# Performance work log

Measured on AMD Instinct MI355X. Metric: run time of the kernel, lower is better.

Reference implementation:

```python
import jax, jax.numpy as jnp
import numpy as np

N = 100000   # nodes
E = 1000000  # edges
DIN = 128    # atom_in_features
DE = 16      # edge_attr_dim
H = 128      # hidden width (preprocess/cheb/postprocess)
K = 3        # Chebyshev order
EPS = 1e-5


def setup_inputs() -> dict:
    key = jax.random.key(0)
    ks = jax.random.split(key, 16)
    s = 0.02
    return {
        "x": jax.random.normal(ks[0], (N, DIN), jnp.float32),
        "edge_index": jax.random.randint(ks[1], (2, E), 0, N),
        "edge_attr": jax.random.normal(ks[2], (E, DE), jnp.float32),
        # AtomEdgeInteraction linear: (DIN+DE) -> H
        "w_int": jax.random.normal(ks[3], (DIN + DE, H), jnp.float32) * s,
        "b_int": jnp.zeros((H,), jnp.float32),
        # preprocess layer 1: Linear + BatchNorm + ReLU
        "w_pre": jax.random.normal(ks[4], (H, H), jnp.float32) * s,
        "b_pre": jnp.zeros((H,), jnp.float32),
        "g_pre": jnp.ones((H,), jnp.float32),
        "be_pre": jnp.zeros((H,), jnp.float32),
        # ChebConv layers: weight [K, in, out] + bias
        "cheb1_w": jax.random.normal(ks[5], (K, H, H), jnp.float32) * s,
        "cheb1_b": jnp.zeros((H,), jnp.float32),
        "cheb2_w": jax.random.normal(ks[6], (K, H, H), jnp.float32) * s,
        "cheb2_b": jnp.zeros((H,), jnp.float32),
        # postprocess: Linear + BatchNorm + ReLU
        "w_post": jax.random.normal(ks[7], (H, H), jnp.float32) * s,
        "b_post": jnp.zeros((H,), jnp.float32),
        "g_post": jnp.ones((H,), jnp.float32),
        "be_post": jnp.zeros((H,), jnp.float32),
        # output layer H -> 1
        "w_out": jax.random.normal(ks[8], (H, 1), jnp.float32) * s,
        "b_out": jnp.zeros((1,), jnp.float32),
    }


def _bn(z, g, b):
    # BatchNorm1d, training-mode batch statistics (biased variance, like torch)
    m = z.mean(0)
    v = ((z - m) ** 2).mean(0)
    return g * (z - m) * jax.lax.rsqrt(v + EPS) + b


def _cheb(h, W, b, row, col, norm):
    # ChebConv with sym normalization, lambda_max=2 => L_hat = -D^{-1/2} A D^{-1/2}
    def lhat(z):
        return jax.ops.segment_sum(norm[:, None] * z[row], col, num_segments=N)

    Tx0 = h
    out = Tx0 @ W[0]
    Tx1 = lhat(Tx0)
    out = out + Tx1 @ W[1]
    for k in range(2, W.shape[0]):
        Tx2 = 2.0 * lhat(Tx1) - Tx0
        out = out + Tx2 @ W[k]
        Tx0, Tx1 = Tx1, Tx2
    return out + b


def reference(x, edge_index, edge_attr,
              w_int, b_int,
              w_pre, b_pre, g_pre, be_pre,
              cheb1_w, cheb1_b, cheb2_w, cheb2_b,
              w_post, b_post, g_post, be_post,
              w_out, b_out):
    row, col = edge_index[0], edge_index[1]
    ones_e = jnp.ones((E,), x.dtype)

    # AtomEdgeInteraction: gather -> concat -> linear -> scatter_mean over col
    comb = jnp.concatenate([x[row], edge_attr], axis=-1)  # [E, DIN+DE]
    upd = comb @ w_int + b_int                             # [E, H]
    cnt = jax.ops.segment_sum(ones_e, col, num_segments=N)
    h = jax.ops.segment_sum(upd, col, num_segments=N) / jnp.clip(cnt, 1.0)[:, None]

    # preprocess layer 1 (Linear + BN + ReLU; dropout rate 0)
    h = jax.nn.relu(_bn(h @ w_pre + b_pre, g_pre, be_pre))

    # sym-normalized edge coefficients for scaled Laplacian
    deg = jax.ops.segment_sum(ones_e, row, num_segments=N)
    dis = jnp.where(deg > 0, jax.lax.rsqrt(jnp.maximum(deg, 1.0)), 0.0)
    norm = -dis[row] * dis[col]  # [E]

    h = jax.nn.relu(_cheb(h, cheb1_w, cheb1_b, row, col, norm))
    h = jax.nn.relu(_cheb(h, cheb2_w, cheb2_b, row, col, norm))

    # postprocess (Linear + BN + ReLU)
    h = jax.nn.relu(_bn(h @ w_post + b_post, g_post, be_post))

    # output layer, squeeze(-1) -> [N]
    return (h @ w_out + b_out).squeeze(-1)
```

## Files before the change

### kernel.cpp

```cpp
#include <hip/hip_runtime.h>
#include <hip/hip_bf16.h>

using u16 = unsigned short;
using u32 = unsigned int;

#define NN 100000
#define NE 1000000

typedef __attribute__((ext_vector_type(8))) short bfrag;
typedef __attribute__((ext_vector_type(4))) float ffrag;

#define BF16ONE2 0x3F803F80u

__device__ __forceinline__ float bf2f(u16 u) { return __uint_as_float(((u32)u) << 16); }
__device__ __forceinline__ u16 f2bf(float f) {
  u32 x = __float_as_uint(f);
  return (u16)((x + 0x7fffu + ((x >> 16) & 1u)) >> 16);
}
__device__ __forceinline__ float rdv(const void* p, long i, int f) {
  return f ? bf2f(((const u16*)p)[i]) : ((const float*)p)[i];
}
__device__ __forceinline__ void acc8(float* a, uint4 v, float w) {
  a[0] = fmaf(w, __uint_as_float(v.x << 16), a[0]);
  a[1] = fmaf(w, __uint_as_float(v.x & 0xffff0000u), a[1]);
  a[2] = fmaf(w, __uint_as_float(v.y << 16), a[2]);
  a[3] = fmaf(w, __uint_as_float(v.y & 0xffff0000u), a[3]);
  a[4] = fmaf(w, __uint_as_float(v.z << 16), a[4]);
  a[5] = fmaf(w, __uint_as_float(v.z & 0xffff0000u), a[5]);
  a[6] = fmaf(w, __uint_as_float(v.w << 16), a[6]);
  a[7] = fmaf(w, __uint_as_float(v.w & 0xffff0000u), a[7]);
}

#define OWXT 0
#define OWPRE 16384
#define OWD1 32768
#define OW11 49152
#define OV21 65536
#define OWD2 81920
#define OW12 98304
#define OV22 114688
#define OWPOST 131072
#define OWET 147456

struct PrepArgs { const void* in[16]; };

__global__ void k_prep(PrepArgs a, const u32* __restrict__ gp, u16* __restrict__ wq,
                       float* __restrict__ wf) {
  int t = blockIdx.x * 256 + threadIdx.x;
  int f = (gp[0] == BF16ONE2) ? 1 : 0;
  if (t < 16384) {
    int o = t >> 7, k = t & 127;
    int ko = k * 128 + o;
    int ok = o * 128 + k;
    wq[OWXT + ok] = f2bf(rdv(a.in[0], ko, f));
    wq[OWPRE + ok] = f2bf(rdv(a.in[2], ko, f));
    float c0 = rdv(a.in[6], ko, f);
    float c1 = rdv(a.in[6], 16384 + ko, f);
    float c2 = rdv(a.in[6], 32768 + ko, f);
    wq[OWD1 + ok] = f2bf(c0 - c2);
    wq[OW11 + ok] = f2bf(c1);
    wq[OV21 + ok] = f2bf(2.f * c2);
    float d0 = rdv(a.in[8], ko, f);
    float d1 = rdv(a.in[8], 16384 + ko, f);
    float d2 = rdv(a.in[8], 32768 + ko, f);
    wq[OWD2 + ok] = f2bf(d0 - d2);
    wq[OW12 + ok] = f2bf(d1);
    wq[OV22 + ok] = f2bf(2.f * d2);
    wq[OWPOST + ok] = f2bf(rdv(a.in[10], ko, f));
  }
  if (t < 4096) {
    int o = t >> 5, k = t & 31;
    wq[OWET + o * 32 + k] = (k < 16) ? f2bf(rdv(a.in[0], (long)(128 + k) * 128 + o, f)) : (u16)0;
  }
  if (t < 1281) {
    int s = t >> 7, j = t & 127;
    const int map[11] = {1, 3, 4, 5, 7, 9, 11, 12, 13, 14, 15};
    wf[t] = rdv(a.in[map[s]], j, f);
  }
}

__global__ void k_hist(const int* __restrict__ ei, int* cnt, int* deg) {
  int e = blockIdx.x * 256 + threadIdx.x;
  if (e >= NE) return;
  atomicAdd(&deg[ei[e]], 1);
  atomicAdd(&cnt[ei[NE + e]], 1);
}

__global__ void k_scan1(const int* __restrict__ cnt, int* off, int* bsum) {
  __shared__ int s[1024];
  int t = threadIdx.x;
  int g = blockIdx.x * 1024 + t;
  int v = (g < NN) ? cnt[g] : 0;
  s[t] = v;
  __syncthreads();
  for (int st = 1; st < 1024; st <<= 1) {
    int x = (t >= st) ? s[t - st] : 0;
    __syncthreads();
    s[t] += x;
    __syncthreads();
  }
  if (g < NN) off[g] = s[t] - v;
  if (t == 1023) bsum[blockIdx.x] = s[t];
}

__global__ void k_scan23(int* off, const int* __restrict__ bsum,
                         const int* __restrict__ deg, float* __restrict__ dis, int nb) {
  __shared__ int s[128];
  int t = threadIdx.x;
  int v = 0;
  if (t < 128) {
    v = (t < nb) ? bsum[t] : 0;
    s[t] = v;
  }
  __syncthreads();
  for (int st = 1; st < 128; st <<= 1) {
    int x = (t >= st && t < 128) ? s[t - st] : 0;
    __syncthreads();
    if (t < 128) s[t] += x;
    __syncthreads();
  }
  if (t < 128) s[t] -= v;
  __syncthreads();
  int pre = s[blockIdx.x];
  int g = blockIdx.x * 1024 + t;
  if (g < NN) {
    off[g] += pre;
    int d = deg[g];
    dis[g] = d > 0 ? rsqrtf((float)d) : 0.f;
  }
  if (g == 0) off[NN] = NE;
}

__global__ void k_place(const int* __restrict__ ei, const int* __restrict__ off,
                        int* cur, int* crow, int* ceid) {
  int e = blockIdx.x * 256 + threadIdx.x;
  if (e >= NE) return;
  int r = ei[e], c = ei[NE + e];
  int p = off[c] + atomicAdd(&cur[c], 1);
  crow[p] = r;
  ceid[p] = e;
}

__global__ __launch_bounds__(256) void k_spmm(const u16* __restrict__ src,
                                              u16* __restrict__ dst,
                                              const int* __restrict__ off,
                                              const int* __restrict__ crow,
                                              const float* __restrict__ cnorm,
                                              const u16* __restrict__ G, int relu) {
  int t = threadIdx.x;
  int node = blockIdx.x * 8 + (t >> 5);
  if (node >= NN) return;
  int l = t & 31;
  int half = l >> 4;
  int c = (l & 15) * 8;
  int p0 = off[node], p1 = off[node + 1];
  float a[8];
#pragma unroll
  for (int j = 0; j < 8; j++) a[j] = 0.f;
  const u16* sp = src + c;
  if (cnorm) {
    int p = p0 + half;
    for (; p + 6 < p1; p += 8) {
      int r0 = crow[p], r1 = crow[p + 2], r2 = crow[p + 4], r3 = crow[p + 6];
      float w0 = cnorm[p], w1 = cnorm[p + 2], w2 = cnorm[p + 4], w3 = cnorm[p + 6];
      uint4 v0 = *(const uint4*)(sp + (long)r0 * 128);
      uint4 v1 = *(const uint4*)(sp + (long)r1 * 128);
      uint4 v2 = *(const uint4*)(sp + (long)r2 * 128);
      uint4 v3 = *(const uint4*)(sp + (long)r3 * 128);
      acc8(a, v0, w0);
      acc8(a, v1, w1);
      acc8(a, v2, w2);
      acc8(a, v3, w3);
    }
    for (; p < p1; p += 2) {
      acc8(a, *(const uint4*)(sp + (long)crow[p] * 128), cnorm[p]);
    }
  } else {
    int p = p0 + half;
    for (; p + 6 < p1; p += 8) {
      int r0 = crow[p], r1 = crow[p + 2], r2 = crow[p + 4], r3 = crow[p + 6];
      uint4 v0 = *(const uint4*)(sp + (long)r0 * 128);
      uint4 v1 = *(const uint4*)(sp + (long)r1 * 128);
      uint4 v2 = *(const uint4*)(sp + (long)r2 * 128);
      uint4 v3 = *(const uint4*)(sp + (long)r3 * 128);
      acc8(a, v0, 1.f);
      acc8(a, v1, 1.f);
      acc8(a, v2, 1.f);
      acc8(a, v3, 1.f);
    }
    for (; p < p1; p += 2) acc8(a, *(const uint4*)(sp + (long)crow[p] * 128), 1.f);
  }
#pragma unroll
  for (int j = 0; j < 8; j++) a[j] += __shfl_xor(a[j], 16);
  if (half) return;
  if (G) acc8(a, *(const uint4*)(G + (long)node * 128 + c), 1.f);
  if (relu) {
#pragma unroll
    for (int j = 0; j < 8; j++) a[j] = fmaxf(a[j], 0.f);
  }
  uint4 o;
  o.x = (u32)f2bf(a[0]) | ((u32)f2bf(a[1]) << 16);
  o.y = (u32)f2bf(a[2]) | ((u32)f2bf(a[3]) << 16);
  o.z = (u32)f2bf(a[4]) | ((u32)f2bf(a[5]) << 16);
  o.w = (u32)f2bf(a[6]) | ((u32)f2bf(a[7]) << 16);
  *(uint4*)(dst + (long)node * 128 + c) = o;
}

__global__ __launch_bounds__(256) void k_asum(const void* __restrict__ eattr,
                                              const u32* __restrict__ gp,
                                              u16* __restrict__ asum,
                                              const int* __restrict__ off,
                                              const int* __restrict__ ceid,
                                              const int* __restrict__ crow,
                                              const float* __restrict__ dis,
                                              float* __restrict__ cnorm) {
  int t = blockIdx.x * 256 + threadIdx.x;
  int node = t >> 4;
  if (node >= NN) return;
  int j = t & 15;
  int p0 = off[node], p1 = off[node + 1];
  float ndis = -dis[node];
  for (int p = p0 + j; p < p1; p += 16) cnorm[p] = ndis * dis[crow[p]];
  float a = 0.f;
  if (gp[0] == BF16ONE2) {
    const u16* e16 = (const u16*)eattr;
    int p = p0;
    for (; p + 4 <= p1; p += 4) {
      float v0 = bf2f(e16[(long)ceid[p] * 16 + j]);
      float v1 = bf2f(e16[(long)ceid[p + 1] * 16 + j]);
      float v2 = bf2f(e16[(long)ceid[p + 2] * 16 + j]);
      float v3 = bf2f(e16[(long)ceid[p + 3] * 16 + j]);
      a += v0 + v1 + v2 + v3;
    }
    for (; p < p1; p++) a += bf2f(e16[(long)ceid[p] * 16 + j]);
  } else {
    const float* e32 = (const float*)eattr;
    int p = p0;
    for (; p + 4 <= p1; p += 4) {
      float v0 = e32[(long)ceid[p] * 16 + j];
      float v1 = e32[(long)ceid[p + 1] * 16 + j];
      float v2 = e32[(long)ceid[p + 2] * 16 + j];
      float v3 = e32[(long)ceid[p + 3] * 16 + j];
      a += v0 + v1 + v2 + v3;
    }
    for (; p < p1; p++) a += e32[(long)ceid[p] * 16 + j];
  }
  asum[(long)node * 16 + j] = f2bf(a);
}

struct MArgs {
  const void* A0; const u16* W0T; int a0raw;
  const u16* A1; const u16* W1T;
  const u16* W2T; u16* out2;
  const float* bias;
  u16* out;
  const u32* gp;
  float* part;
};

#define ASTRIDE 136
#define ESTRIDE 132

template <int DUAL, int K0, int ROWS>
__global__ __launch_bounds__(256) void k_mgemm(MArgs m) {
  constexpr int RT = ROWS / 16;
  constexpr int TPR = 256 / ROWS;
  constexpr int SEGW = K0 / TPR;
  constexpr int NKB0 = K0 / 32;
  __shared__ __align__(16) u16 sA[ROWS * ASTRIDE];
  int tid = threadIdx.x;
  int wv = tid >> 6, lane = tid & 63;
  int col16 = lane & 15, quad = lane >> 4;
  int r0 = blockIdx.x * ROWS;

  ffrag acc[RT * 2];
#pragma unroll
  for (int i = 0; i < RT * 2; i++)
#pragma unroll
    for (int g = 0; g < 4; g++) acc[i][g] = 0.f;

  {
    int row = tid / TPR, seg = tid % TPR;
    int ra = r0 + row;
    if (ra >= NN) ra = NN - 1;
    bool f32a = m.a0raw && (m.gp[0] != BF16ONE2);
    if (f32a) {
      const float* gs = (const float*)m.A0 + (long)ra * K0 + seg * SEGW;
      u32* lp = (u32*)(sA + row * ASTRIDE + seg * SEGW);
#pragma unroll
      for (int e = 0; e < SEGW / 8; e++) {
        float4 v0 = *(const float4*)(gs + e * 8);
        float4 v1 = *(const float4*)(gs + e * 8 + 4);
        lp[e * 4 + 0] = (u32)f2bf(v0.x) | ((u32)f2bf(v0.y) << 16);
        lp[e * 4 + 1] = (u32)f2bf(v0.z) | ((u32)f2bf(v0.w) << 16);
        lp[e * 4 + 2] = (u32)f2bf(v1.x) | ((u32)f2bf(v1.y) << 16);
        lp[e * 4 + 3] = (u32)f2bf(v1.z) | ((u32)f2bf(v1.w) << 16);
      }
    } else {
      const u16* gs = (const u16*)m.A0 + (long)ra * K0 + seg * SEGW;
      uint4* lp = (uint4*)(sA + row * ASTRIDE + seg * SEGW);
#pragma unroll
      for (int e = 0; e < SEGW / 8; e++) lp[e] = *(const uint4*)(gs + e * 8);
    }
  }
  bfrag b0[2][NKB0];
#pragma unroll
  for (int c = 0; c < 2; c++)
#pragma unroll
    for (int kb = 0; kb < NKB0; kb++)
      b0[c][kb] = *(const bfrag*)(m.W0T + (long)(wv * 32 + c * 16 + col16) * K0 + kb * 32 + quad * 8);
  __syncthreads();
#pragma unroll
  for (int kb = 0; kb < NKB0; kb++)
#pragma unroll
    for (int rt = 0; rt < RT; rt++) {
      bfrag af = *(const bfrag*)(sA + (rt * 16 + col16) * ASTRIDE + kb * 32 + quad * 8);
      acc[rt * 2 + 0] = __builtin_amdgcn_mfma_f32_16x16x32_bf16(af, b0[0][kb], acc[rt * 2 + 0], 0, 0, 0);
      acc[rt * 2 + 1] = __builtin_amdgcn_mfma_f32_16x16x32_bf16(af, b0[1][kb], acc[rt * 2 + 1], 0, 0, 0);
    }

  ffrag acc2[DUAL ? RT * 2 : 1];
  if constexpr (DUAL) {
#pragma unroll
    for (int i = 0; i < RT * 2; i++)
#pragma unroll
      for (int g = 0; g < 4; g++) acc2[i][g] = 0.f;
    __syncthreads();
    {
      int row = tid / TPR, seg = tid % TPR;
      int ra = r0 + row;
      if (ra >= NN) ra = NN - 1;
      const u16* gs = m.A1 + (long)ra * 128 + seg * SEGW;
      uint4* lp = (uint4*)(sA + row * ASTRIDE + seg * SEGW);
#pragma unroll
      for (int e = 0; e < SEGW / 8; e++) lp[e] = *(const uint4*)(gs + e * 8);
    }
    bfrag b1[2][4], b2[2][4];
#pragma unroll
    for (int c = 0; c < 2; c++)
#pragma unroll
      for (int kb = 0; kb < 4; kb++) {
        b1[c][kb] = *(const bfrag*)(m.W1T + (long)(wv * 32 + c * 16 + col16) * 128 + kb * 32 + quad * 8);
        b2[c][kb] = *(const bfrag*)(m.W2T + (long)(wv * 32 + c * 16 + col16) * 128 + kb * 32 + quad * 8);
      }
    __syncthreads();
#pragma unroll
    for (int kb = 0; kb < 4; kb++)
#pragma unroll
      for (int rt = 0; rt < RT; rt++) {
        bfrag af = *(const bfrag*)(sA + (rt * 16 + col16) * ASTRIDE + kb * 32 + quad * 8);
        acc[rt * 2 + 0] = __builtin_amdgcn_mfma_f32_16x16x32_bf16(af, b1[0][kb], acc[rt * 2 + 0], 0, 0, 0);
        acc[rt * 2 + 1] = __builtin_amdgcn_mfma_f32_16x16x32_bf16(af, b1[1][kb], acc[rt * 2 + 1], 0, 0, 0);
        acc2[rt * 2 + 0] = __builtin_amdgcn_mfma_f32_16x16x32_bf16(af, b2[0][kb], acc2[rt * 2 + 0], 0, 0, 0);
        acc2[rt * 2 + 1] = __builtin_amdgcn_mfma_f32_16x16x32_bf16(af, b2[1][kb], acc2[rt * 2 + 1], 0, 0, 0);
      }
  }

  __syncthreads();
#pragma unroll
  for (int rt = 0; rt < RT; rt++)
#pragma unroll
    for (int c = 0; c < 2; c++) {
      int col = wv * 32 + c * 16 + col16;
      float bj = m.bias ? m.bias[col] : 0.f;
#pragma unroll
      for (int g = 0; g < 4; g++)
        sA[(rt * 16 + quad * 4 + g) * ESTRIDE + col] = f2bf(acc[rt * 2 + c][g] + bj);
    }
  __syncthreads();
  {
    constexpr int CPT = 128 / TPR;
    int rr = tid / TPR, d = tid % TPR;
    int rowg = r0 + rr;
    if (rowg < NN) {
      const u16* sp2 = sA + rr * ESTRIDE + d * CPT;
      uint4* o = (uint4*)(m.out + (long)rowg * 128 + d * CPT);
#pragma unroll
      for (int e = 0; e < CPT / 8; e++) {
        const uint2* s2 = (const uint2*)(sp2 + e * 8);
        uint2 lo = s2[0], hi = s2[1];
        o[e] = make_uint4(lo.x, lo.y, hi.x, hi.y);
      }
    }
  }
  if (m.part) {
    __shared__ float ps[256], pq[256];
    int col = tid & 127, hf = tid >> 7;
    float s = 0.f, q = 0.f;
#pragma unroll
    for (int r = 0; r < ROWS / 2; r++) {
      int rr = hf * (ROWS / 2) + r;
      if (r0 + rr < NN) {
        float v = bf2f(sA[rr * ESTRIDE + col]);
        s += v;
        q += v * v;
      }
    }
    ps[tid] = s;
    pq[tid] = q;
    __syncthreads();
    if (tid < 128) {
      m.part[(long)blockIdx.x * 256 + tid] = ps[tid] + ps[tid + 128];
      m.part[(long)blockIdx.x * 256 + 128 + tid] = pq[tid] + pq[tid + 128];
    }
  }
  if constexpr (DUAL) {
    __syncthreads();
#pragma unroll
    for (int rt = 0; rt < RT; rt++)
#pragma unroll
      for (int c = 0; c < 2; c++) {
        int col = wv * 32 + c * 16 + col16;
#pragma unroll
        for (int g = 0; g < 4; g++)
          sA[(rt * 16 + quad * 4 + g) * ESTRIDE + col] = f2bf(acc2[rt * 2 + c][g]);
      }
    __syncthreads();
    constexpr int CPT = 128 / TPR;
    int rr = tid / TPR, d = tid % TPR;
    int rowg = r0 + rr;
    if (rowg < NN) {
      const u16* sp2 = sA + rr * ESTRIDE + d * CPT;
      uint4* o = (uint4*)(m.out2 + (long)rowg * 128 + d * CPT);
#pragma unroll
      for (int e = 0; e < CPT / 8; e++) {
        const uint2* s2 = (const uint2*)(sp2 + e * 8);
        uint2 lo = s2[0], hi = s2[1];
        o[e] = make_uint4(lo.x, lo.y, hi.x, hi.y);
      }
    }
  }
}

__global__ __launch_bounds__(256) void k_etpre(const u16* __restrict__ asum,
                                               const u16* __restrict__ Wet,
                                               const u16* __restrict__ Wpre,
                                               const float* __restrict__ b_int,
                                               const float* __restrict__ b_pre,
                                               const u16* __restrict__ G,
                                               const int* __restrict__ cnt,
                                               u16* __restrict__ out, float* part) {
  __shared__ __align__(16) u16 sA[64 * ASTRIDE];
  int tid = threadIdx.x;
  int wv = tid >> 6, lane = tid & 63;
  int col16 = lane & 15, quad = lane >> 4;
  int r0 = blockIdx.x * 64;

  {
    int row = tid >> 2, seg = tid & 3;
    int ra = r0 + row;
    if (ra >= NN) ra = NN - 1;
    if (seg < 2) {
      *(uint4*)(sA + row * ASTRIDE + seg * 8) = *(const uint4*)(asum + (long)ra * 16 + seg * 8);
    } else {
      *(uint4*)(sA + row * ASTRIDE + seg * 8) = make_uint4(0, 0, 0, 0);
    }
  }
  bfrag be[2];
#pragma unroll
  for (int c = 0; c < 2; c++)
    be[c] = *(const bfrag*)(Wet + (long)(wv * 32 + c * 16 + col16) * 32 + quad * 8);
  __syncthreads();
  ffrag acc[8];
#pragma unroll
  for (int i = 0; i < 8; i++)
#pragma unroll
    for (int g = 0; g < 4; g++) acc[i][g] = 0.f;
#pragma unroll
  for (int rt = 0; rt < 4; rt++) {
    bfrag af = *(const bfrag*)(sA + (rt * 16 + col16) * ASTRIDE + quad * 8);
    acc[rt * 2 + 0] = __builtin_amdgcn_mfma_f32_16x16x32_bf16(af, be[0], acc[rt * 2 + 0], 0, 0, 0);
    acc[rt * 2 + 1] = __builtin_amdgcn_mfma_f32_16x16x32_bf16(af, be[1], acc[rt * 2 + 1], 0, 0, 0);
  }
  __syncthreads();
#pragma unroll
  for (int rt = 0; rt < 4; rt++)
#pragma unroll
    for (int c = 0; c < 2; c++) {
      int col = wv * 32 + c * 16 + col16;
      float bj = b_int[col];
#pragma unroll
      for (int g = 0; g < 4; g++) {
        int r = r0 + rt * 16 + quad * 4 + g;
        float v = acc[rt * 2 + c][g];
        int cc = 0;
        if (r < NN) {
          v += bf2f(G[(long)r * 128 + col]);
          cc = cnt[r];
        }
        v = (v + (float)cc * bj) / (float)(cc > 1 ? cc : 1);
        sA[(rt * 16 + quad * 4 + g) * ASTRIDE + col] = f2bf(v);
      }
    }
  bfrag b1[2][4];
#pragma unroll
  for (int c = 0; c < 2; c++)
#pragma unroll
    for (int kb = 0; kb < 4; kb++)
      b1[c][kb] = *(const bfrag*)(Wpre + (long)(wv * 32 + c * 16 + col16) * 128 + kb * 32 + quad * 8);
  __syncthreads();
  ffrag a2[8];
#pragma unroll
  for (int i = 0; i < 8; i++)
#pragma unroll
    for (int g = 0; g < 4; g++) a2[i][g] = 0.f;
#pragma unroll
  for (int kb = 0; kb < 4; kb++)
#pragma unroll
    for (int rt = 0; rt < 4; rt++) {
      bfrag af = *(const bfrag*)(sA + (rt * 16 + col16) * ASTRIDE + kb * 32 + quad * 8);
      a2[rt * 2 + 0] = __builtin_amdgcn_mfma_f32_16x16x32_bf16(af, b1[0][kb], a2[rt * 2 + 0], 0, 0, 0);
      a2[rt * 2 + 1] = __builtin_amdgcn_mfma_f32_16x16x32_bf16(af, b1[1][kb], a2[rt * 2 + 1], 0, 0, 0);
    }
  __syncthreads();
#pragma unroll
  for (int rt = 0; rt < 4; rt++)
#pragma unroll
    for (int c = 0; c < 2; c++) {
      int col = wv * 32 + c * 16 + col16;
      float bj = b_pre[col];
#pragma unroll
      for (int g = 0; g < 4; g++)
        sA[(rt * 16 + quad * 4 + g) * ESTRIDE + col] = f2bf(a2[rt * 2 + c][g] + bj);
    }
  __syncthreads();
  {
    int rr = tid >> 2, d = tid & 3;
    int rowg = r0 + rr;
    if (rowg < NN) {
      const u16* sp2 = sA + rr * ESTRIDE + d * 32;
      uint4* o = (uint4*)(out + (long)rowg * 128 + d * 32);
#pragma unroll
      for (int e = 0; e < 4; e++) {
        const uint2* s2 = (const uint2*)(sp2 + e * 8);
        uint2 lo = s2[0], hi = s2[1];
        o[e] = make_uint4(lo.x, lo.y, hi.x, hi.y);
      }
    }
  }
  {
    __shared__ float ps[256], pq[256];
    int col = tid & 127, hf = tid >> 7;
    float s = 0.f, q = 0.f;
#pragma unroll
    for (int r = 0; r < 32; r++) {
      int rr = hf * 32 + r;
      if (r0 + rr < NN) {
        float v = bf2f(sA[rr * ESTRIDE + col]);
        s += v;
        q += v * v;
      }
    }
    ps[tid] = s;
    pq[tid] = q;
    __syncthreads();
    if (tid < 128) {
      part[(long)blockIdx.x * 256 + tid] = ps[tid] + ps[tid + 128];
      part[(long)blockIdx.x * 256 + 128 + tid] = pq[tid] + pq[tid + 128];
    }
  }
}

__global__ void k_redfin(const float* __restrict__ part, const float* __restrict__ gamma,
                         const float* __restrict__ beta, float* ab, int nblk) {
  int tid = threadIdx.x;
  int col = blockIdx.x * 16 + (tid & 15);
  int ch = tid >> 4;
  float s = 0.f, q = 0.f;
  for (int b = ch; b < nblk; b += 16) {
    s += part[(long)b * 256 + col];
    q += part[(long)b * 256 + 128 + col];
  }
  __shared__ float sh[256], qh[256];
  sh[tid] = s;
  qh[tid] = q;
  __syncthreads();
  if (tid < 16) {
    float ts = 0.f, tq = 0.f;
#pragma unroll
    for (int i = 0; i < 16; i++) {
      ts += sh[i * 16 + tid];
      tq += qh[i * 16 + tid];
    }
    int j = blockIdx.x * 16 + tid;
    float m = ts * (1.f / (float)NN);
    float v = fmaxf(tq * (1.f / (float)NN) - m * m, 0.f);
    float a = gamma[j] * rsqrtf(v + 1e-5f);
    ab[j] = a;
    ab[128 + j] = beta[j] - m * a;
  }
}

__global__ void k_bnrelu(const u16* __restrict__ z, u16* __restrict__ out,
                         const float* __restrict__ ab) {
  long idx = (long)blockIdx.x * 256 + threadIdx.x;
  long t = idx * 2;
  if (t >= (long)NN * 128) return;
  int col = (int)(t & 127);
  u32 v = *(const u32*)(z + t);
  float f0 = fmaxf(__uint_as_float(v << 16) * ab[col] + ab[128 + col], 0.f);
  float f1 = fmaxf(__uint_as_float(v & 0xffff0000u) * ab[col + 1] + ab[129 + col], 0.f);
  *(u32*)(out + t) = (u32)f2bf(f0) | ((u32)f2bf(f1) << 16);
}

__global__ void k_out(const u16* __restrict__ z, const float* __restrict__ ab,
                      const float* __restrict__ wout, const float* __restrict__ bout,
                      const u32* __restrict__ gp, void* __restrict__ y) {
  int node = blockIdx.x * 4 + (threadIdx.x >> 6);
  if (node >= NN) return;
  int lane = threadIdx.x & 63;
  float s = 0.f;
#pragma unroll
  for (int c = lane; c < 128; c += 64) {
    float zz = bf2f(z[(long)node * 128 + c]);
    float h = fmaxf(ab[c] * zz + ab[128 + c], 0.f);
    s += h * wout[c];
  }
#pragma unroll
  for (int o = 32; o > 0; o >>= 1) s += __shfl_down(s, o);
  if (lane == 0) {
    float r = s + bout[0];
    if (gp[0] == BF16ONE2) ((u16*)y)[node] = f2bf(r);
    else ((float*)y)[node] = r;
  }
}

extern "C" void kernel_launch(void* const* d_in, const int* in_sizes, int n_in,
                              void* d_out, int out_size, void* d_ws, size_t ws_size,
                              hipStream_t stream) {
  const void* x = d_in[0];
  const int* ei = (const int*)d_in[1];
  const void* eattr = d_in[2];
  const u32* gp = (const u32*)d_in[7];
  (void)in_sizes; (void)n_in; (void)out_size; (void)ws_size;

  char* w = (char*)d_ws;
  size_t p = 0;
  auto alloc = [&](size_t b) { size_t r = p; p += (b + 255) & ~(size_t)255; return r; };
  size_t o_cnt = alloc((size_t)NN * 4);
  size_t o_deg = alloc((size_t)NN * 4);
  size_t o_cur = alloc((size_t)NN * 4);
  size_t o_zero_end = p;
  size_t o_dis = alloc((size_t)NN * 4);
  size_t o_off = alloc((size_t)(NN + 1) * 4);
  size_t o_bsum = alloc(1024 * 4);
  size_t o_ab = alloc(512 * 4);
  size_t o_wq = alloc((size_t)151552 * 2);
  size_t o_wf = alloc((size_t)1281 * 4);
  size_t o_crow = alloc((size_t)NE * 4);
  size_t o_cnrm = alloc((size_t)NE * 4);
  size_t o_asum = alloc((size_t)NN * 16 * 2);
  size_t o_part = alloc((size_t)1563 * 256 * 4);
  size_t o_Bx = alloc((size_t)NN * 128 * 2);
  size_t o_Bt = alloc((size_t)NN * 128 * 2);

  int* cnt = (int*)(w + o_cnt);
  int* deg = (int*)(w + o_deg);
  int* cur = (int*)(w + o_cur);
  float* dis = (float*)(w + o_dis);
  int* off = (int*)(w + o_off);
  int* bsum = (int*)(w + o_bsum);
  float* abA = (float*)(w + o_ab);
  float* abB = abA + 256;
  u16* wq = (u16*)(w + o_wq);
  float* wf = (float*)(w + o_wf);
  int* crow = (int*)(w + o_crow);
  float* cnrm = (float*)(w + o_cnrm);
  u16* asum = (u16*)(w + o_asum);
  float* part = (float*)(w + o_part);
  u16* Bx = (u16*)(w + o_Bx);
  u16* Bt = (u16*)(w + o_Bt);
  int* ceid = (int*)Bt;

  hipMemsetAsync(w + o_cnt, 0, o_zero_end - o_cnt, stream);

  int gE = (NE + 255) / 256;
  int nb = (NN + 1023) / 1024;
  int gS = (NN + 7) / 8;
  int gG1 = (NN + 127) / 128;
  int gG2 = (NN + 63) / 64;

  {
    PrepArgs a;
    for (int i = 0; i < 16; i++) a.in[i] = d_in[3 + i];
    k_prep<<<64, 256, 0, stream>>>(a, gp, wq, wf);
  }

  k_hist<<<gE, 256, 0, stream>>>(ei, cnt, deg);
  k_scan1<<<nb, 1024, 0, stream>>>(cnt, off, bsum);
  k_scan23<<<nb, 1024, 0, stream>>>(off, bsum, deg, dis, nb);
  k_place<<<gE, 256, 0, stream>>>(ei, off, cur, crow, ceid);
  k_asum<<<(NN * 16 + 255) / 256, 256, 0, stream>>>(eattr, gp, asum, off, ceid, crow, dis, cnrm);

  {
    MArgs a = {};
    a.A0 = x; a.W0T = wq + OWXT; a.a0raw = 1;
    a.out = Bx; a.gp = gp;
    k_mgemm<0, 128, 128><<<gG1, 256, 0, stream>>>(a);
  }
  k_spmm<<<gS, 256, 0, stream>>>(Bx, Bt, off, crow, nullptr, nullptr, 0);
  k_etpre<<<gG2, 256, 0, stream>>>(asum, wq + OWET, wq + OWPRE, wf + 0, wf + 128,
                                   Bt, cnt, Bt, part);
  k_redfin<<<8, 256, 0, stream>>>(part, wf + 256, wf + 384, abA, gG2);
  k_bnrelu<<<(int)(((long)NN * 128 / 2 + 255) / 256), 256, 0, stream>>>(Bt, Bx, abA);

  k_spmm<<<gS, 256, 0, stream>>>(Bx, Bt, off, crow, cnrm, nullptr, 0);
  {
    MArgs a = {};
    a.A0 = Bx; a.W0T = wq + OWD1;
    a.A1 = Bt; a.W1T = wq + OW11;
    a.W2T = wq + OV21; a.out2 = Bt;
    a.bias = wf + 512; a.out = Bx; a.gp = gp;
    k_mgemm<1, 128, 64><<<gG2, 256, 0, stream>>>(a);
  }
  k_spmm<<<gS, 256, 0, stream>>>(Bt, Bx, off, crow, cnrm, Bx, 1);

  k_spmm<<<gS, 256, 0, stream>>>(Bx, Bt, off, crow, cnrm, nullptr, 0);
  {
    MArgs a = {};
    a.A0 = Bx; a.W0T = wq + OWD2;
    a.A1 = Bt; a.W1T = wq + OW12;
    a.W2T = wq + OV22; a.out2 = Bt;
    a.bias = wf + 640; a.out = Bx; a.gp = gp;
    k_mgemm<1, 128, 64><<<gG2, 256, 0, stream>>>(a);
  }
  k_spmm<<<gS, 256, 0, stream>>>(Bt, Bx, off, crow, cnrm, Bx, 1);

  {
    MArgs a = {};
    a.A0 = Bx; a.W0T = wq + OWPOST;
    a.bias = wf + 768; a.out = Bt; a.gp = gp; a.part = part;
    k_mgemm<0, 128, 128><<<gG1, 256, 0, stream>>>(a);
  }
  k_redfin<<<8, 256, 0, stream>>>(part, wf + 896, wf + 1024, abB, gG1);
  k_out<<<(NN + 3) / 4, 256, 0, stream>>>(Bt, abB, wf + 1152, wf + 1280, gp, d_out);
}
```

Baseline: 809.6 us.

## Fuse neighbor gather into Chebyshev and preprocess GEMM kernels

The sparse aggregation is moved inside the GEMM kernels. A new gather_lds helper accumulates neighbor rows straight into shared memory: unweighted for the interaction step in k_etpre, and weighted by cnorm for the second Chebyshev term in the new k_cheb. k_cheb takes the place of the earlier pattern of a dual GEMM, a write of an intermediate T1@W2 product, and a second gather with bias and relu. This removes one standalone sparse-aggregation launch per Chebyshev layer and one for the interaction step, along with their intermediate round trips through global memory. In exchange, each 16-thread group gathers four nodes one after another inside a GEMM-shaped block, which may lower memory-level parallelism for the irregular loads.

```diff
diff --git a/kernel.cpp b/kernel.cpp
--- a/kernel.cpp
+++ b/kernel.cpp
@@ -41,6 +41,9 @@
 #define OV22 114688
 #define OWPOST 131072
 #define OWET 147456
+
+#define ASTRIDE 136
+#define ESTRIDE 132
 
 struct PrepArgs { const void* in[16]; };
 
@@ -145,8 +148,7 @@
                                               u16* __restrict__ dst,
                                               const int* __restrict__ off,
                                               const int* __restrict__ crow,
-                                              const float* __restrict__ cnorm,
-                                              const u16* __restrict__ G, int relu) {
+                                              const float* __restrict__ cnorm) {
   int t = threadIdx.x;
   int node = blockIdx.x * 8 + (t >> 5);
   if (node >= NN) return;
@@ -158,52 +160,75 @@
 #pragma unroll
   for (int j = 0; j < 8; j++) a[j] = 0.f;
   const u16* sp = src + c;
-  if (cnorm) {
-    int p = p0 + half;
-    for (; p + 6 < p1; p += 8) {
-      int r0 = crow[p], r1 = crow[p + 2], r2 = crow[p + 4], r3 = crow[p + 6];
-      float w0 = cnorm[p], w1 = cnorm[p + 2], w2 = cnorm[p + 4], w3 = cnorm[p + 6];
-      uint4 v0 = *(const uint4*)(sp + (long)r0 * 128);
-      uint4 v1 = *(const uint4*)(sp + (long)r1 * 128);
-      uint4 v2 = *(const uint4*)(sp + (long)r2 * 128);
-      uint4 v3 = *(const uint4*)(sp + (long)r3 * 128);
-      acc8(a, v0, w0);
-      acc8(a, v1, w1);
-      acc8(a, v2, w2);
-      acc8(a, v3, w3);
-    }
-    for (; p < p1; p += 2) {
-      acc8(a, *(const uint4*)(sp + (long)crow[p] * 128), cnorm[p]);
-    }
-  } else {
-    int p = p0 + half;
-    for (; p + 6 < p1; p += 8) {
-      int r0 = crow[p], r1 = crow[p + 2], r2 = crow[p + 4], r3 = crow[p + 6];
-      uint4 v0 = *(const uint4*)(sp + (long)r0 * 128);
-      uint4 v1 = *(const uint4*)(sp + (long)r1 * 128);
-      uint4 v2 = *(const uint4*)(sp + (long)r2 * 128);
-      uint4 v3 = *(const uint4*)(sp + (long)r3 * 128);
-      acc8(a, v0, 1.f);
-      acc8(a, v1, 1.f);
-      acc8(a, v2, 1.f);
-      acc8(a, v3, 1.f);
-    }
-    for (; p < p1; p += 2) acc8(a, *(const uint4*)(sp + (long)crow[p] * 128), 1.f);
-  }
+  int p = p0 + half;
+  for (; p + 6 < p1; p += 8) {
+    int r0 = crow[p], r1 = crow[p + 2], r2 = crow[p + 4], r3 = crow[p + 6];
+    float w0 = cnorm[p], w1 = cnorm[p + 2], w2 = cnorm[p + 4], w3 = cnorm[p + 6];
+    uint4 v0 = *(const uint4*)(sp + (long)r0 * 128);
+    uint4 v1 = *(const uint4*)(sp + (long)r1 * 128);
+    uint4 v2 = *(const uint4*)(sp + (long)r2 * 128);
+    uint4 v3 = *(const uint4*)(sp + (long)r3 * 128);
+    acc8(a, v0, w0);
+    acc8(a, v1, w1);
+    acc8(a, v2, w2);
+    acc8(a, v3, w3);
+  }
+  for (; p < p1; p += 2) acc8(a, *(const uint4*)(sp + (long)crow[p] * 128), cnorm[p]);
 #pragma unroll
   for (int j = 0; j < 8; j++) a[j] += __shfl_xor(a[j], 16);
   if (half) return;
-  if (G) acc8(a, *(const uint4*)(G + (long)node * 128 + c), 1.f);
-  if (relu) {
-#pragma unroll
-    for (int j = 0; j < 8; j++) a[j] = fmaxf(a[j], 0.f);
-  }
   uint4 o;
   o.x = (u32)f2bf(a[0]) | ((u32)f2bf(a[1]) << 16);
   o.y = (u32)f2bf(a[2]) | ((u32)f2bf(a[3]) << 16);
   o.z = (u32)f2bf(a[4]) | ((u32)f2bf(a[5]) << 16);
   o.w = (u32)f2bf(a[6]) | ((u32)f2bf(a[7]) << 16);
   *(uint4*)(dst + (long)node * 128 + c) = o;
+}
+
+template <int WEIGHTED>
+__device__ __forceinline__ void gather_lds(u16* sA, const u16* __restrict__ src,
+                                           const int* __restrict__ off,
+                                           const int* __restrict__ crow,
+                                           const float* __restrict__ cnorm, int r0) {
+  int tid = threadIdx.x;
+  int grp = tid >> 4;
+  int c = (tid & 15) * 8;
+  const u16* sp = src + c;
+#pragma unroll
+  for (int i = 0; i < 4; i++) {
+    int nl = grp * 4 + i;
+    int node = r0 + nl;
+    float a[8];
+#pragma unroll
+    for (int j = 0; j < 8; j++) a[j] = 0.f;
+    if (node < NN) {
+      int p0 = off[node], p1 = off[node + 1];
+      int p = p0;
+      for (; p + 4 <= p1; p += 4) {
+        int r0i = crow[p], r1i = crow[p + 1], r2i = crow[p + 2], r3i = crow[p + 3];
+        float w0 = WEIGHTED ? cnorm[p] : 1.f;
+        float w1 = WEIGHTED ? cnorm[p + 1] : 1.f;
+        float w2 = WEIGHTED ? cnorm[p + 2] : 1.f;
+        float w3 = WEIGHTED ? cnorm[p + 3] : 1.f;
+        uint4 v0 = *(const uint4*)(sp + (long)r0i * 128);
+        uint4 v1 = *(const uint4*)(sp + (long)r1i * 128);
+        uint4 v2 = *(const uint4*)(sp + (long)r2i * 128);
+        uint4 v3 = *(const uint4*)(sp + (long)r3i * 128);
+        acc8(a, v0, w0);
+        acc8(a, v1, w1);
+        acc8(a, v2, w2);
+        acc8(a, v3, w3);
+      }
+      for (; p < p1; p++)
+        acc8(a, *(const uint4*)(sp + (long)crow[p] * 128), WEIGHTED ? cnorm[p] : 1.f);
+    }
+    uint4 o;
+    o.x = (u32)f2bf(a[0]) | ((u32)f2bf(a[1]) << 16);
+    o.y = (u32)f2bf(a[2]) | ((u32)f2bf(a[3]) << 16);
+    o.z = (u32)f2bf(a[4]) | ((u32)f2bf(a[5]) << 16);
+    o.w = (u32)f2bf(a[6]) | ((u32)f2bf(a[7]) << 16);
+    *(uint4*)(sA + nl * ASTRIDE + c) = o;
+  }
 }
 
 __global__ __launch_bounds__(256) void k_asum(const void* __restrict__ eattr,
@@ -250,23 +275,14 @@
 
 struct MArgs {
   const void* A0; const u16* W0T; int a0raw;
-  const u16* A1; const u16* W1T;
-  const u16* W2T; u16* out2;
   const float* bias;
   u16* out;
   const u32* gp;
   float* part;
 };
 
-#define ASTRIDE 136
-#define ESTRIDE 132
-
-template <int DUAL, int K0, int ROWS>
 __global__ __launch_bounds__(256) void k_mgemm(MArgs m) {
-  constexpr int RT = ROWS / 16;
-  constexpr int TPR = 256 / ROWS;
-  constexpr int SEGW = K0 / TPR;
-  constexpr int NKB0 = K0 / 32;
+  constexpr int ROWS = 128, RT = 8, TPR = 2, SEGW = 64;
   __shared__ __align__(16) u16 sA[ROWS * ASTRIDE];
   int tid = threadIdx.x;
   int wv = tid >> 6, lane = tid & 63;
@@ -285,7 +301,7 @@
     if (ra >= NN) ra = NN - 1;
     bool f32a = m.a0raw && (m.gp[0] != BF16ONE2);
     if (f32a) {
-      const float* gs = (const float*)m.A0 + (long)ra * K0 + seg * SEGW;
+      const float* gs = (const float*)m.A0 + (long)ra * 128 + seg * SEGW;
       u32* lp = (u32*)(sA + row * ASTRIDE + seg * SEGW);
 #pragma unroll
       for (int e = 0; e < SEGW / 8; e++) {
@@ -297,65 +313,27 @@
         lp[e * 4 + 3] = (u32)f2bf(v1.z) | ((u32)f2bf(v1.w) << 16);
       }
     } else {
-      const u16* gs = (const u16*)m.A0 + (long)ra * K0 + seg * SEGW;
+      const u16* gs = (const u16*)m.A0 + (long)ra * 128 + seg * SEGW;
       uint4* lp = (uint4*)(sA + row * ASTRIDE + seg * SEGW);
 #pragma unroll
       for (int e = 0; e < SEGW / 8; e++) lp[e] = *(const uint4*)(gs + e * 8);
     }
   }
-  bfrag b0[2][NKB0];
+  bfrag b0[2][4];
 #pragma unroll
   for (int c = 0; c < 2; c++)
 #pragma unroll
-    for (int kb = 0; kb < NKB0; kb++)
-      b0[c][kb] = *(const bfrag*)(m.W0T + (long)(wv * 32 + c * 16 + col16) * K0 + kb * 32 + quad * 8);
-  __syncthreads();
-#pragma unroll
-  for (int kb = 0; kb < NKB0; kb++)
+    for (int kb = 0; kb < 4; kb++)
+      b0[c][kb] = *(const bfrag*)(m.W0T + (long)(wv * 32 + c * 16 + col16) * 128 + kb * 32 + quad * 8);
+  __syncthreads();
+#pragma unroll
+  for (int kb = 0; kb < 4; kb++)
 #pragma unroll
     for (int rt = 0; rt < RT; rt++) {
       bfrag af = *(const bfrag*)(sA + (rt * 16 + col16) * ASTRIDE + kb * 32 + quad * 8);
       acc[rt * 2 + 0] = __builtin_amdgcn_mfma_f32_16x16x32_bf16(af, b0[0][kb], acc[rt * 2 + 0], 0, 0, 0);
       acc[rt * 2 + 1] = __builtin_amdgcn_mfma_f32_16x16x32_bf16(af, b0[1][kb], acc[rt * 2 + 1], 0, 0, 0);
     }
-
-  ffrag acc2[DUAL ? RT * 2 : 1];
-  if constexpr (DUAL) {
-#pragma unroll
-    for (int i = 0; i < RT * 2; i++)
-#pragma unroll
-      for (int g = 0; g < 4; g++) acc2[i][g] = 0.f;
-    __syncthreads();
-    {
-      int row = tid / TPR, seg = tid % TPR;
-      int ra = r0 + row;
-      if (ra >= NN) ra = NN - 1;
-      const u16* gs = m.A1 + (long)ra * 128 + seg * SEGW;
-      uint4* lp = (uint4*)(sA + row * ASTRIDE + seg * SEGW);
-#pragma unroll
-      for (int e = 0; e < SEGW / 8; e++) lp[e] = *(const uint4*)(gs + e * 8);
-    }
-    bfrag b1[2][4], b2[2][4];
-#pragma unroll
-    for (int c = 0; c < 2; c++)
-#pragma unroll
-      for (int kb = 0; kb < 4; kb++) {
-        b1[c][kb] = *(const bfrag*)(m.W1T + (long)(wv * 32 + c * 16 + col16) * 128 + kb * 32 + quad * 8);
-        b2[c][kb] = *(const bfrag*)(m.W2T + (long)(wv * 32 + c * 16 + col16) * 128 + kb * 32 + quad * 8);
-      }
-    __syncthreads();
-#pragma unroll
-    for (int kb = 0; kb < 4; kb++)
-#pragma unroll
-      for (int rt = 0; rt < RT; rt++) {
-        bfrag af = *(const bfrag*)(sA + (rt * 16 + col16) * ASTRIDE + kb * 32 + quad * 8);
-        acc[rt * 2 + 0] = __builtin_amdgcn_mfma_f32_16x16x32_bf16(af, b1[0][kb], acc[rt * 2 + 0], 0, 0, 0);
-        acc[rt * 2 + 1] = __builtin_amdgcn_mfma_f32_16x16x32_bf16(af, b1[1][kb], acc[rt * 2 + 1], 0, 0, 0);
-        acc2[rt * 2 + 0] = __builtin_amdgcn_mfma_f32_16x16x32_bf16(af, b2[0][kb], acc2[rt * 2 + 0], 0, 0, 0);
-        acc2[rt * 2 + 1] = __builtin_amdgcn_mfma_f32_16x16x32_bf16(af, b2[1][kb], acc2[rt * 2 + 1], 0, 0, 0);
-      }
-  }
-
   __syncthreads();
 #pragma unroll
   for (int rt = 0; rt < RT; rt++)
@@ -369,14 +347,13 @@
     }
   __syncthreads();
   {
-    constexpr int CPT = 128 / TPR;
     int rr = tid / TPR, d = tid % TPR;
     int rowg = r0 + rr;
     if (rowg < NN) {
-      const u16* sp2 = sA + rr * ESTRIDE + d * CPT;
-      uint4* o = (uint4*)(m.out + (long)rowg * 128 + d * CPT);
-#pragma unroll
-      for (int e = 0; e < CPT / 8; e++) {
+      const u16* sp2 = sA + rr * ESTRIDE + d * 64;
+      uint4* o = (uint4*)(m.out + (long)rowg * 128 + d * 64);
+#pragma unroll
+      for (int e = 0; e < 8; e++) {
         const uint2* s2 = (const uint2*)(sp2 + e * 8);
         uint2 lo = s2[0], hi = s2[1];
         o[e] = make_uint4(lo.x, lo.y, hi.x, hi.y);
@@ -388,8 +365,8 @@
     int col = tid & 127, hf = tid >> 7;
     float s = 0.f, q = 0.f;
 #pragma unroll
-    for (int r = 0; r < ROWS / 2; r++) {
-      int rr = hf * (ROWS / 2) + r;
+    for (int r = 0; r < 64; r++) {
+      int rr = hf * 64 + r;
       if (r0 + rr < NN) {
         float v = bf2f(sA[rr * ESTRIDE + col]);
         s += v;
@@ -404,40 +381,16 @@
       m.part[(long)blockIdx.x * 256 + 128 + tid] = pq[tid] + pq[tid + 128];
     }
   }
-  if constexpr (DUAL) {
-    __syncthreads();
-#pragma unroll
-    for (int rt = 0; rt < RT; rt++)
-#pragma unroll
-      for (int c = 0; c < 2; c++) {
-        int col = wv * 32 + c * 16 + col16;
-#pragma unroll
-        for (int g = 0; g < 4; g++)
-          sA[(rt * 16 + quad * 4 + g) * ESTRIDE + col] = f2bf(acc2[rt * 2 + c][g]);
-      }
-    __syncthreads();
-    constexpr int CPT = 128 / TPR;
-    int rr = tid / TPR, d = tid % TPR;
-    int rowg = r0 + rr;
-    if (rowg < NN) {
-      const u16* sp2 = sA + rr * ESTRIDE + d * CPT;
-      uint4* o = (uint4*)(m.out2 + (long)rowg * 128 + d * CPT);
-#pragma unroll
-      for (int e = 0; e < CPT / 8; e++) {
-        const uint2* s2 = (const uint2*)(sp2 + e * 8);
-        uint2 lo = s2[0], hi = s2[1];
-        o[e] = make_uint4(lo.x, lo.y, hi.x, hi.y);
-      }
-    }
-  }
-}
-
-__global__ __launch_bounds__(256) void k_etpre(const u16* __restrict__ asum,
+}
+
+__global__ __launch_bounds__(256) void k_etpre(const u16* __restrict__ Xg,
+                                               const u16* __restrict__ asum,
                                                const u16* __restrict__ Wet,
                                                const u16* __restrict__ Wpre,
                                                const float* __restrict__ b_int,
                                                const float* __restrict__ b_pre,
-                                               const u16* __restrict__ G,
+                                               const int* __restrict__ off,
+                                               const int* __restrict__ crow,
                                                const int* __restrict__ cnt,
                                                u16* __restrict__ out, float* part) {
   __shared__ __align__(16) u16 sA[64 * ASTRIDE];
@@ -450,28 +403,29 @@
     int row = tid >> 2, seg = tid & 3;
     int ra = r0 + row;
     if (ra >= NN) ra = NN - 1;
-    if (seg < 2) {
+    if (seg < 2)
       *(uint4*)(sA + row * ASTRIDE + seg * 8) = *(const uint4*)(asum + (long)ra * 16 + seg * 8);
-    } else {
+    else
       *(uint4*)(sA + row * ASTRIDE + seg * 8) = make_uint4(0, 0, 0, 0);
-    }
   }
   bfrag be[2];
 #pragma unroll
   for (int c = 0; c < 2; c++)
     be[c] = *(const bfrag*)(Wet + (long)(wv * 32 + c * 16 + col16) * 32 + quad * 8);
   __syncthreads();
-  ffrag acc[8];
+  ffrag accE[8];
 #pragma unroll
   for (int i = 0; i < 8; i++)
 #pragma unroll
-    for (int g = 0; g < 4; g++) acc[i][g] = 0.f;
+    for (int g = 0; g < 4; g++) accE[i][g] = 0.f;
 #pragma unroll
   for (int rt = 0; rt < 4; rt++) {
     bfrag af = *(const bfrag*)(sA + (rt * 16 + col16) * ASTRIDE + quad * 8);
-    acc[rt * 2 + 0] = __builtin_amdgcn_mfma_f32_16x16x32_bf16(af, be[0], acc[rt * 2 + 0], 0, 0, 0);
-    acc[rt * 2 + 1] = __builtin_amdgcn_mfma_f32_16x16x32_bf16(af, be[1], acc[rt * 2 + 1], 0, 0, 0);
-  }
+    accE[rt * 2 + 0] = __builtin_amdgcn_mfma_f32_16x16x32_bf16(af, be[0], accE[rt * 2 + 0], 0, 0, 0);
+    accE[rt * 2 + 1] = __builtin_amdgcn_mfma_f32_16x16x32_bf16(af, be[1], accE[rt * 2 + 1], 0, 0, 0);
+  }
+  __syncthreads();
+  gather_lds<0>(sA, Xg, off, crow, nullptr, r0);
   __syncthreads();
 #pragma unroll
   for (int rt = 0; rt < 4; rt++)
@@ -481,15 +435,12 @@
       float bj = b_int[col];
 #pragma unroll
       for (int g = 0; g < 4; g++) {
-        int r = r0 + rt * 16 + quad * 4 + g;
-        float v = acc[rt * 2 + c][g];
-        int cc = 0;
-        if (r < NN) {
-          v += bf2f(G[(long)r * 128 + col]);
-          cc = cnt[r];
-        }
+        int rr = rt * 16 + quad * 4 + g;
+        int r = r0 + rr;
+        float v = accE[rt * 2 + c][g] + bf2f(sA[rr * ASTRIDE + col]);
+        int cc = (r < NN) ? cnt[r] : 0;
         v = (v + (float)cc * bj) / (float)(cc > 1 ? cc : 1);
-        sA[(rt * 16 + quad * 4 + g) * ASTRIDE + col] = f2bf(v);
+        sA[rr * ASTRIDE + col] = f2bf(v);
       }
     }
   bfrag b1[2][4];
@@ -557,6 +508,123 @@
     if (tid < 128) {
       part[(long)blockIdx.x * 256 + tid] = ps[tid] + ps[tid + 128];
       part[(long)blockIdx.x * 256 + 128 + tid] = pq[tid] + pq[tid + 128];
+    }
+  }
+}
+
+__global__ __launch_bounds__(256) void k_cheb(const u16* __restrict__ hb,
+                                              const u16* __restrict__ T1,
+                                              const int* __restrict__ off,
+                                              const int* __restrict__ crow,
+                                              const float* __restrict__ cnorm,
+                                              const u16* __restrict__ WD,
+                                              const u16* __restrict__ W1,
+                                              const u16* __restrict__ V2,
+                                              const float* __restrict__ bias,
+                                              u16* __restrict__ out) {
+  __shared__ __align__(16) u16 sA[64 * ASTRIDE];
+  int tid = threadIdx.x;
+  int wv = tid >> 6, lane = tid & 63;
+  int col16 = lane & 15, quad = lane >> 4;
+  int r0 = blockIdx.x * 64;
+
+  ffrag acc[8];
+#pragma unroll
+  for (int i = 0; i < 8; i++)
+#pragma unroll
+    for (int g = 0; g < 4; g++) acc[i][g] = 0.f;
+
+  gather_lds<1>(sA, T1, off, crow, cnorm, r0);
+  bfrag bv[2][4];
+#pragma unroll
+  for (int c = 0; c < 2; c++)
+#pragma unroll
+    for (int kb = 0; kb < 4; kb++)
+      bv[c][kb] = *(const bfrag*)(V2 + (long)(wv * 32 + c * 16 + col16) * 128 + kb * 32 + quad * 8);
+  __syncthreads();
+#pragma unroll
+  for (int kb = 0; kb < 4; kb++)
+#pragma unroll
+    for (int rt = 0; rt < 4; rt++) {
+      bfrag af = *(const bfrag*)(sA + (rt * 16 + col16) * ASTRIDE + kb * 32 + quad * 8);
+      acc[rt * 2 + 0] = __builtin_amdgcn_mfma_f32_16x16x32_bf16(af, bv[0][kb], acc[rt * 2 + 0], 0, 0, 0);
+      acc[rt * 2 + 1] = __builtin_amdgcn_mfma_f32_16x16x32_bf16(af, bv[1][kb], acc[rt * 2 + 1], 0, 0, 0);
+    }
+  __syncthreads();
+
+  {
+    int row = tid >> 2, seg = tid & 3;
+    int ra = r0 + row;
+    if (ra >= NN) ra = NN - 1;
+    const u16* gs = hb + (long)ra * 128 + seg * 32;
+    uint4* lp = (uint4*)(sA + row * ASTRIDE + seg * 32);
+#pragma unroll
+    for (int e = 0; e < 4; e++) lp[e] = *(const uint4*)(gs + e * 8);
+  }
+#pragma unroll
+  for (int c = 0; c < 2; c++)
+#pragma unroll
+    for (int kb = 0; kb < 4; kb++)
+      bv[c][kb] = *(const bfrag*)(WD + (long)(wv * 32 + c * 16 + col16) * 128 + kb * 32 + quad * 8);
+  __syncthreads();
+#pragma unroll
+  for (int kb = 0; kb < 4; kb++)
+#pragma unroll
+    for (int rt = 0; rt < 4; rt++) {
+      bfrag af = *(const bfrag*)(sA + (rt * 16 + col16) * ASTRIDE + kb * 32 + quad * 8);
+      acc[rt * 2 + 0] = __builtin_amdgcn_mfma_f32_16x16x32_bf16(af, bv[0][kb], acc[rt * 2 + 0], 0, 0, 0);
+      acc[rt * 2 + 1] = __builtin_amdgcn_mfma_f32_16x16x32_bf16(af, bv[1][kb], acc[rt * 2 + 1], 0, 0, 0);
+    }
+  __syncthreads();
+
+  {
+    int row = tid >> 2, seg = tid & 3;
+    int ra = r0 + row;
+    if (ra >= NN) ra = NN - 1;
+    const u16* gs = T1 + (long)ra * 128 + seg * 32;
+    uint4* lp = (uint4*)(sA + row * ASTRIDE + seg * 32);
+#pragma unroll
+    for (int e = 0; e < 4; e++) lp[e] = *(const uint4*)(gs + e * 8);
+  }
+#pragma unroll
+  for (int c = 0; c < 2; c++)
+#pragma unroll
+    for (int kb = 0; kb < 4; kb++)
+      bv[c][kb] = *(const bfrag*)(W1 + (long)(wv * 32 + c * 16 + col16) * 128 + kb * 32 + quad * 8);
+  __syncthreads();
+#pragma unroll
+  for (int kb = 0; kb < 4; kb++)
+#pragma unroll
+    for (int rt = 0; rt < 4; rt++) {
+      bfrag af = *(const bfrag*)(sA + (rt * 16 + col16) * ASTRIDE + kb * 32 + quad * 8);
+      acc[rt * 2 + 0] = __builtin_amdgcn_mfma_f32_16x16x32_bf16(af, bv[0][kb], acc[rt * 2 + 0], 0, 0, 0);
+      acc[rt * 2 + 1] = __builtin_amdgcn_mfma_f32_16x16x32_bf16(af, bv[1][kb], acc[rt * 2 + 1], 0, 0, 0);
+    }
+  __syncthreads();
+
+#pragma unroll
+  for (int rt = 0; rt < 4; rt++)
+#pragma unroll
+    for (int c = 0; c < 2; c++) {
+      int col = wv * 32 + c * 16 + col16;
+      float bj = bias[col];
+#pragma unroll
+      for (int g = 0; g < 4; g++)
+        sA[(rt * 16 + quad * 4 + g) * ESTRIDE + col] = f2bf(fmaxf(acc[rt * 2 + c][g] + bj, 0.f));
+    }
+  __syncthreads();
+  {
+    int rr = tid >> 2, d = tid & 3;
+    int rowg = r0 + rr;
+    if (rowg < NN) {
+      const u16* sp2 = sA + rr * ESTRIDE + d * 32;
+      uint4* o = (uint4*)(out + (long)rowg * 128 + d * 32);
+#pragma unroll
+      for (int e = 0; e < 4; e++) {
+        const uint2* s2 = (const uint2*)(sp2 + e * 8);
+        uint2 lo = s2[0], hi = s2[1];
+        o[e] = make_uint4(lo.x, lo.y, hi.x, hi.y);
+      }
     }
   }
 }
@@ -696,41 +764,26 @@
     MArgs a = {};
     a.A0 = x; a.W0T = wq + OWXT; a.a0raw = 1;
     a.out = Bx; a.gp = gp;
-    k_mgemm<0, 128, 128><<<gG1, 256, 0, stream>>>(a);
-  }
-  k_spmm<<<gS, 256, 0, stream>>>(Bx, Bt, off, crow, nullptr, nullptr, 0);
-  k_etpre<<<gG2, 256, 0, stream>>>(asum, wq + OWET, wq + OWPRE, wf + 0, wf + 128,
-                                   Bt, cnt, Bt, part);
+    k_mgemm<<<gG1, 256, 0, stream>>>(a);
+  }
+  k_etpre<<<gG2, 256, 0, stream>>>(Bx, asum, wq + OWET, wq + OWPRE, wf + 0, wf + 128,
+                                   off, crow, cnt, Bt, part);
   k_redfin<<<8, 256, 0, stream>>>(part, wf + 256, wf + 384, abA, gG2);
   k_bnrelu<<<(int)(((long)NN * 128 / 2 + 255) / 256), 256, 0, stream>>>(Bt, Bx, abA);
 
-  k_spmm<<<gS, 256, 0, stream>>>(Bx, Bt, off, crow, cnrm, nullptr, 0);
-  {
-    MArgs a = {};
-    a.A0 = Bx; a.W0T = wq + OWD1;
-    a.A1 = Bt; a.W1T = wq + OW11;
-    a.W2T = wq + OV21; a.out2 = Bt;
-    a.bias = wf + 512; a.out = Bx; a.gp = gp;
-    k_mgemm<1, 128, 64><<<gG2, 256, 0, stream>>>(a);
-  }
-  k_spmm<<<gS, 256, 0, stream>>>(Bt, Bx, off, crow, cnrm, Bx, 1);
-
-  k_spmm<<<gS, 256, 0, stream>>>(Bx, Bt, off, crow, cnrm, nullptr, 0);
-  {
-    MArgs a = {};
-    a.A0 = Bx; a.W0T = wq + OWD2;
-    a.A1 = Bt; a.W1T = wq + OW12;
-    a.W2T = wq + OV22; a.out2 = Bt;
-    a.bias = wf + 640; a.out = Bx; a.gp = gp;
-    k_mgemm<1, 128, 64><<<gG2, 256, 0, stream>>>(a);
-  }
-  k_spmm<<<gS, 256, 0, stream>>>(Bt, Bx, off, crow, cnrm, Bx, 1);
+  k_spmm<<<gS, 256, 0, stream>>>(Bx, Bt, off, crow, cnrm);
+  k_cheb<<<gG2, 256, 0, stream>>>(Bx, Bt, off, crow, cnrm,
+                                  wq + OWD1, wq + OW11, wq + OV21, wf + 512, Bx);
+
+  k_spmm<<<gS, 256, 0, stream>>>(Bx, Bt, off, crow, cnrm);
+  k_cheb<<<gG2, 256, 0, stream>>>(Bx, Bt, off, crow, cnrm,
+                                  wq + OWD2, wq + OW12, wq + OV22, wf + 640, Bx);
 
   {
     MArgs a = {};
     a.A0 = Bx; a.W0T = wq + OWPOST;
     a.bias = wf + 768; a.out = Bt; a.gp = gp; a.part = part;
-    k_mgemm<0, 128, 128><<<gG1, 256, 0, stream>>>(a);
+    k_mgemm<<<gG1, 256, 0, stream>>>(a);
   }
   k_redfin<<<8, 256, 0, stream>>>(part, wf + 896, wf + 1024, abB, gG1);
   k_out<<<(NN + 3) / 4, 256, 0, stream>>>(Bt, abB, wf + 1152, wf + 1280, gp, d_out);
```

Measured after the change: 759.0 us. 1.07x faster.
